# Kernel tuning notes

Measured on AMD Instinct MI355X. Metric: run time of the kernel, lower is better.

The kernel has to match this reference:

```python
import jax, jax.numpy as jnp
from jax import lax
import numpy as np
import math

NUM_CLASSES = 81
N_PER_IMG = 1024
NUM_IMAGES = 8
SCORE_THRESH = 0.05
NMS_THRESH = 0.5
DETS_PER_IMG = 100
WX, WY, WW, WH = 10.0, 10.0, 5.0, 5.0
BBOX_XFORM_CLIP = math.log(1000.0 / 16.0)


def setup_inputs() -> dict:
    key = jax.random.key(0)
    k1, k2, k3, k4 = jax.random.split(key, 4)
    M = NUM_IMAGES * N_PER_IMG
    H, W = 800, 1333
    class_logits = jax.random.normal(k1, (M, NUM_CLASSES), dtype=jnp.float32) * 3.0
    box_regression = jax.random.normal(k2, (M, 4 * NUM_CLASSES), dtype=jnp.float32) * 0.5
    # valid xyxy proposals inside the image
    xy1 = jax.random.uniform(k3, (M, 2), dtype=jnp.float32) * jnp.array([W * 0.7, H * 0.7], jnp.float32)
    wh = jax.random.uniform(k4, (M, 2), dtype=jnp.float32) * jnp.array([W * 0.3, H * 0.3], jnp.float32) + 4.0
    proposals = jnp.concatenate([xy1, xy1 + wh], axis=1)
    return {"class_logits": class_logits, "box_regression": box_regression,
            "proposals": proposals, "height": H, "width": W}


def _decode(rel_codes, boxes):
    widths = boxes[:, 2] - boxes[:, 0] + 1.0
    heights = boxes[:, 3] - boxes[:, 1] + 1.0
    ctr_x = boxes[:, 0] + 0.5 * widths
    ctr_y = boxes[:, 1] + 0.5 * heights
    rel = rel_codes.reshape(rel_codes.shape[0], -1, 4)  # [M, C, 4]
    dx = rel[:, :, 0] / WX
    dy = rel[:, :, 1] / WY
    dw = jnp.minimum(rel[:, :, 2] / WW, BBOX_XFORM_CLIP)
    dh = jnp.minimum(rel[:, :, 3] / WH, BBOX_XFORM_CLIP)
    pctr_x = dx * widths[:, None] + ctr_x[:, None]
    pctr_y = dy * heights[:, None] + ctr_y[:, None]
    pw = jnp.exp(dw) * widths[:, None]
    ph = jnp.exp(dh) * heights[:, None]
    return jnp.stack([pctr_x - 0.5 * pw, pctr_y - 0.5 * ph,
                      pctr_x + 0.5 * pw - 1.0, pctr_y + 0.5 * ph - 1.0], axis=-1)


def _clip(boxes, height, width):
    # boxes [..., 4] xyxy, clamp to [0, W-1] x [0, H-1]
    x = jnp.clip(boxes[..., 0::2], 0.0, float(width - 1))
    y = jnp.clip(boxes[..., 1::2], 0.0, float(height - 1))
    return jnp.stack([x[..., 0], y[..., 0], x[..., 1], y[..., 1]], axis=-1)


def _iou_matrix(b):
    x1, y1, x2, y2 = b[:, 0], b[:, 1], b[:, 2], b[:, 3]
    area = (x2 - x1 + 1.0) * (y2 - y1 + 1.0)
    xx1 = jnp.maximum(x1[:, None], x1[None, :])
    yy1 = jnp.maximum(y1[:, None], y1[None, :])
    xx2 = jnp.minimum(x2[:, None], x2[None, :])
    yy2 = jnp.minimum(y2[:, None], y2[None, :])
    inter = jnp.clip(xx2 - xx1 + 1.0, 0.0) * jnp.clip(yy2 - yy1 + 1.0, 0.0)
    return inter / (area[:, None] + area[None, :] - inter)


def _per_class(scores_j, boxes_j):
    # scores_j [N], boxes_j [N,4] -> sorted scores/boxes + greedy-NMS keep mask
    N = scores_j.shape[0]
    valid = scores_j > SCORE_THRESH
    s = jnp.where(valid, scores_j, 0.0)  # softmax scores are > 0
    order = jnp.argsort(-s)
    s_sorted = s[order]
    b_sorted = boxes_j[order]
    valid_sorted = valid[order]
    iou = _iou_matrix(b_sorted)  # [N, N]
    idxs = jnp.arange(N)

    def body(i, keep):
        sup = (iou[i] > NMS_THRESH) & keep[i] & (idxs > i)
        return keep & ~sup

    keep = lax.fori_loop(0, N, body, valid_sorted)
    return s_sorted, b_sorted, keep


def _per_image(prob_i, boxes_i):
    # prob_i [N, C], boxes_i [N, C, 4]; skip background class 0
    C = prob_i.shape[1]
    fg_scores = prob_i[:, 1:].T                      # [C-1, N]
    fg_boxes = jnp.swapaxes(boxes_i[:, 1:, :], 0, 1)  # [C-1, N, 4]
    s_sorted, b_sorted, keep = jax.vmap(_per_class)(fg_scores, fg_boxes)
    labels = jnp.broadcast_to(jnp.arange(1, C, dtype=jnp.int32)[:, None], s_sorted.shape)
    flat_s = jnp.where(keep, s_sorted, 0.0).reshape(-1)
    vals, idx = lax.top_k(flat_s, DETS_PER_IMG)      # detections-per-image limit
    boxes_out = b_sorted.reshape(-1, 4)[idx]
    labels_out = labels.reshape(-1)[idx]
    ok = vals > SCORE_THRESH
    return (jnp.where(ok, vals, 0.0),
            jnp.where(ok[:, None], boxes_out, 0.0),
            jnp.where(ok, labels_out, 0))


def reference(class_logits, box_regression, proposals, height, width):
    prob = jax.nn.softmax(class_logits, axis=-1)          # [M, C]
    dec = _decode(box_regression, proposals)              # [M, C, 4]
    dec = _clip(dec, height, width)
    B, N, C = NUM_IMAGES, N_PER_IMG, NUM_CLASSES
    prob = prob.reshape(B, N, C)
    dec = dec.reshape(B, N, C, 4)
    scores, boxes, labels = lax.map(lambda a: _per_image(a[0], a[1]), (prob, dec))
    return scores, boxes, labels
```

## Files before the change

kernel.cpp:

```cpp
#include <hip/hip_runtime.h>
#include <stdint.h>
#include <math.h>

#define NCLS 81
#define NFG  80
#define NPI  1024
#define NIMG 8
#define DETS 100
#define SCORE_T 0.05f
#define NMS_T   0.5f
#define NCAND   (NFG * DETS)
#define CAND_CAP 2048
#define FASTN 256
#define ROWS 64

static constexpr float BBOX_CLIP = 4.1351665567423557f;

__global__ __launch_bounds__(256) void softmax_probT(
    const float* __restrict__ logits, float* __restrict__ probT, int M)
{
    __shared__ float tile[ROWS * NCLS];
    __shared__ float mx[ROWS], dn[ROWS];
    int t = threadIdx.x;
    int rbase = blockIdx.x * ROWS;

    for (int idx = t; idx < ROWS * NCLS; idx += 256)
        tile[idx] = logits[(size_t)rbase * NCLS + idx];
    __syncthreads();

    if (t < ROWS) {
        const float* r = tile + t * NCLS;
        float m = r[0];
        #pragma unroll
        for (int j = 1; j < NCLS; ++j) m = fmaxf(m, r[j]);
        float s = 0.f;
        #pragma unroll
        for (int j = 0; j < NCLS; ++j) s += expf(r[j] - m);
        mx[t] = m; dn[t] = s;
    }
    __syncthreads();

    for (int o = t; o < ROWS * NFG; o += 256) {
        int r = o & 63;
        int c = o >> 6;
        float v = expf(tile[r * NCLS + (c + 1)] - mx[r]) / dn[r];
        probT[(size_t)c * M + rbase + r] = v;
    }
}

__global__ __launch_bounds__(256) void per_class_nms(
    const float* __restrict__ probT, const float* __restrict__ boxreg,
    const float* __restrict__ props, const int* __restrict__ hptr,
    const int* __restrict__ wptr, int* __restrict__ out_cnt,
    float* __restrict__ out_score, unsigned* __restrict__ out_key,
    float* __restrict__ out_box, int M)
{
    int pid = blockIdx.x;
    int img = pid / NFG;
    int c   = pid % NFG;
    int cls = c + 1;

    __shared__ float box_lds[NPI][4];
    __shared__ unsigned long long key[NPI];
    __shared__ int keep[NPI];
    __shared__ float sbox[FASTN][4];
    __shared__ float sarea[FASTN];
    __shared__ unsigned long long mask[FASTN][FASTN/64];
    __shared__ unsigned long long keepw[FASTN/64];
    __shared__ unsigned wpre[4];
    __shared__ int cnt;

    int t = threadIdx.x;
    float W1 = (float)(*wptr - 1);
    float H1 = (float)(*hptr - 1);

    if (t == 0) cnt = 0;
    for (int i = t; i < NPI; i += 256) key[i] = 0ULL;
    __syncthreads();

    {
        const float4 pv = *(const float4*)(probT + (size_t)c * M + img * NPI + 4 * t);
        float pr[4] = {pv.x, pv.y, pv.z, pv.w};
        #pragma unroll
        for (int j = 0; j < 4; ++j) {
            if (pr[j] > SCORE_T) {
                int m = 4 * t + j;
                int g = img * NPI + m;
                const float4 pb = *(const float4*)(props + (size_t)g * 4);
                float x1 = pb.x, y1 = pb.y, x2 = pb.z, y2 = pb.w;
                float w  = x2 - x1 + 1.0f, h = y2 - y1 + 1.0f;
                float cx = x1 + 0.5f * w,  cy = y1 + 0.5f * h;
                const float4 rc = *(const float4*)(boxreg + (size_t)g * (4 * NCLS) + 4 * cls);
                float dx = rc.x / 10.0f, dy = rc.y / 10.0f;
                float dw = fminf(rc.z / 5.0f, BBOX_CLIP);
                float dh = fminf(rc.w / 5.0f, BBOX_CLIP);
                float pcx = dx * w + cx, pcy = dy * h + cy;
                float pw = expf(dw) * w, ph = expf(dh) * h;
                float bx1 = pcx - 0.5f * pw;
                float by1 = pcy - 0.5f * ph;
                float bx2 = pcx + 0.5f * pw - 1.0f;
                float by2 = pcy + 0.5f * ph - 1.0f;
                bx1 = fminf(fmaxf(bx1, 0.f), W1);
                bx2 = fminf(fmaxf(bx2, 0.f), W1);
                by1 = fminf(fmaxf(by1, 0.f), H1);
                by2 = fminf(fmaxf(by2, 0.f), H1);
                box_lds[m][0] = bx1; box_lds[m][1] = by1;
                box_lds[m][2] = bx2; box_lds[m][3] = by2;
                int p = atomicAdd(&cnt, 1);
                unsigned fb = __float_as_uint(pr[j]);
                key[p] = ((unsigned long long)fb << 32) | (unsigned)(NPI - 1 - m);
            }
        }
    }
    __syncthreads();
    int n = cnt;

    if (n <= 64) {
        if (t < 64) {
            int lane = t;
            unsigned long long k = (lane < n) ? key[lane] : 0ULL;
            #pragma unroll
            for (int kk = 2; kk <= 64; kk <<= 1) {
                #pragma unroll
                for (int j = kk >> 1; j > 0; j >>= 1) {
                    unsigned long long o = __shfl_xor(k, j, 64);
                    bool up = ((lane & kk) == 0);
                    bool lower = ((lane & j) == 0);
                    bool take_max = (up == lower);
                    k = take_max ? (k > o ? k : o) : (k < o ? k : o);
                }
            }
            bool valid = (lane < n);
            float bx1 = 0.f, by1 = 0.f, bx2 = 0.f, by2 = 0.f, area = 0.f;
            if (valid) {
                int mi = NPI - 1 - (int)(k & 0xFFFFFFFFu);
                bx1 = box_lds[mi][0]; by1 = box_lds[mi][1];
                bx2 = box_lds[mi][2]; by2 = box_lds[mi][3];
                area = (bx2 - bx1 + 1.f) * (by2 - by1 + 1.f);
            }
            unsigned long long sup = 0ULL;
            for (int i = 0; i < n; ++i) {
                bool alive = !((sup >> i) & 1ULL);
                float ax1 = __shfl(bx1, i, 64), ay1 = __shfl(by1, i, 64);
                float ax2 = __shfl(bx2, i, 64), ay2 = __shfl(by2, i, 64);
                float aarea = __shfl(area, i, 64);
                bool s = false;
                if (alive && valid && lane > i) {
                    float xx1 = fmaxf(ax1, bx1), yy1 = fmaxf(ay1, by1);
                    float xx2 = fminf(ax2, bx2), yy2 = fminf(ay2, by2);
                    float iw = fmaxf(xx2 - xx1 + 1.f, 0.f);
                    float ih = fmaxf(yy2 - yy1 + 1.f, 0.f);
                    float inter = iw * ih;
                    float iou = inter / (aarea + area - inter);
                    s = iou > NMS_T;
                }
                sup |= __ballot(s);
            }
            bool kept = valid && !((sup >> lane) & 1ULL);
            unsigned long long keptm = __ballot(kept);
            int rank = __popcll(keptm & ((1ULL << lane) - 1ULL));
            if (kept && rank < DETS) {
                int slot = pid * DETS + rank;
                out_score[slot] = __uint_as_float((unsigned)(k >> 32));
                out_key[slot] = (unsigned)(c * NPI + lane);
                out_box[slot * 4 + 0] = bx1;
                out_box[slot * 4 + 1] = by1;
                out_box[slot * 4 + 2] = bx2;
                out_box[slot * 4 + 3] = by2;
            }
            if (lane == 0) {
                int tot = __popcll(keptm);
                out_cnt[pid] = tot < DETS ? tot : DETS;
            }
        }
        return;
    }

    int P = 2;
    while (P < n) P <<= 1;
    for (int k = 2; k <= P; k <<= 1) {
        for (int j = k >> 1; j > 0; j >>= 1) {
            for (int i = t; i < P; i += 256) {
                int ixj = i ^ j;
                if (ixj > i) {
                    unsigned long long a = key[i], b = key[ixj];
                    bool up = (i & k) == 0;
                    if (up ? (a < b) : (a > b)) { key[i] = b; key[ixj] = a; }
                }
            }
            __syncthreads();
        }
    }

    for (int i = t; i < NPI; i += 256) keep[i] = 0;
    __syncthreads();

    if (n <= FASTN) {
        for (int i = t; i < n; i += 256) {
            int mi = NPI - 1 - (int)(key[i] & 0xFFFFFFFFu);
            float bx1 = box_lds[mi][0], by1 = box_lds[mi][1];
            float bx2 = box_lds[mi][2], by2 = box_lds[mi][3];
            sbox[i][0] = bx1; sbox[i][1] = by1; sbox[i][2] = bx2; sbox[i][3] = by2;
            sarea[i] = (bx2 - bx1 + 1.f) * (by2 - by1 + 1.f);
        }
        __syncthreads();
        int nwords = ((n + 63) >> 6);
        for (int w = t; w < n * (FASTN/64); w += 256) {
            int i = w >> 2, wb = w & 3;
            if (wb >= nwords || ((wb + 1) << 6) - 1 <= i) { mask[i][wb] = 0ULL; continue; }
            float ax1 = sbox[i][0], ay1 = sbox[i][1];
            float ax2 = sbox[i][2], ay2 = sbox[i][3];
            float aarea = sarea[i];
            unsigned long long bits = 0ULL;
            int jbase = wb << 6;
            #pragma unroll 4
            for (int b = 0; b < 64; ++b) {
                int j = jbase + b;
                if (j < n && j > i) {
                    float bx1 = sbox[j][0], by1 = sbox[j][1];
                    float bx2 = sbox[j][2], by2 = sbox[j][3];
                    float xx1 = fmaxf(ax1, bx1), yy1 = fmaxf(ay1, by1);
                    float xx2 = fminf(ax2, bx2), yy2 = fminf(ay2, by2);
                    float iw = fmaxf(xx2 - xx1 + 1.f, 0.f);
                    float ih = fmaxf(yy2 - yy1 + 1.f, 0.f);
                    float inter = iw * ih;
                    float iou = inter / (aarea + sarea[j] - inter);
                    if (iou > NMS_T) bits |= (1ULL << b);
                }
            }
            mask[i][wb] = bits;
        }
        __syncthreads();
        if (t < 64) {
            int lane = t;
            unsigned long long kb = 0ULL;
            if (lane < 4) {
                int rem = n - (lane << 6);
                if (rem >= 64) kb = ~0ULL;
                else if (rem > 0) kb = (1ULL << rem) - 1ULL;
            }
            unsigned long long rm = 0ULL;
            for (int i = 0; i < n; ++i) {
                unsigned long long rw = __shfl(rm, i >> 6, 64);
                if (!((rw >> (i & 63)) & 1ULL)) {
                    unsigned long long mrow = (lane < 4) ? mask[i][lane] : 0ULL;
                    rm |= mrow;
                }
            }
            if (lane < 4) keepw[lane] = kb & ~rm;
        }
        __syncthreads();
        for (int i = t; i < n; i += 256)
            keep[i] = (int)((keepw[i >> 6] >> (i & 63)) & 1ULL);
        __syncthreads();
    } else {
        for (int i = t; i < n; i += 256) keep[i] = 1;
        __syncthreads();
        for (int i = 0; i < n; ++i) {
            if (keep[i]) {
                unsigned long long ki = key[i];
                int mi = NPI - 1 - (int)(ki & 0xFFFFFFFFu);
                float ax1 = box_lds[mi][0], ay1 = box_lds[mi][1];
                float ax2 = box_lds[mi][2], ay2 = box_lds[mi][3];
                float aarea = (ax2 - ax1 + 1.f) * (ay2 - ay1 + 1.f);
                for (int jj = i + 1 + t; jj < n; jj += 256) {
                    if (keep[jj]) {
                        int mj = NPI - 1 - (int)(key[jj] & 0xFFFFFFFFu);
                        float bx1 = box_lds[mj][0], by1 = box_lds[mj][1];
                        float bx2 = box_lds[mj][2], by2 = box_lds[mj][3];
                        float xx1 = fmaxf(ax1, bx1), yy1 = fmaxf(ay1, by1);
                        float xx2 = fminf(ax2, bx2), yy2 = fminf(ay2, by2);
                        float iw = fmaxf(xx2 - xx1 + 1.f, 0.f);
                        float ih = fmaxf(yy2 - yy1 + 1.f, 0.f);
                        float inter = iw * ih;
                        float barea = (bx2 - bx1 + 1.f) * (by2 - by1 + 1.f);
                        float iou = inter / (aarea + barea - inter);
                        if (iou > NMS_T) keep[jj] = 0;
                    }
                }
            }
            __syncthreads();
        }
    }

    {
        int lane = t & 63, w = t >> 6;
        int k0 = keep[4 * t], k1 = keep[4 * t + 1];
        int k2 = keep[4 * t + 2], k3 = keep[4 * t + 3];
        unsigned s = (unsigned)(k0 + k1 + k2 + k3);
        unsigned v = s;
        #pragma unroll
        for (int off = 1; off < 64; off <<= 1) {
            unsigned u = __shfl_up(v, off, 64);
            v += (lane >= off) ? u : 0u;
        }
        if (lane == 63) wpre[w] = v;
        __syncthreads();
        unsigned woff = 0;
        for (int w2 = 0; w2 < w; ++w2) woff += wpre[w2];
        unsigned before = v + woff - s;
        unsigned r = before;
        #pragma unroll
        for (int j = 0; j < 4; ++j) {
            int i = 4 * t + j;
            int kv = (j == 0) ? k0 : (j == 1) ? k1 : (j == 2) ? k2 : k3;
            if (kv && r < DETS) {
                unsigned long long ki = key[i];
                int mi = NPI - 1 - (int)(ki & 0xFFFFFFFFu);
                int slot = pid * DETS + (int)r;
                out_score[slot] = __uint_as_float((unsigned)(ki >> 32));
                out_key[slot] = (unsigned)(c * NPI + i);
                out_box[slot * 4 + 0] = box_lds[mi][0];
                out_box[slot * 4 + 1] = box_lds[mi][1];
                out_box[slot * 4 + 2] = box_lds[mi][2];
                out_box[slot * 4 + 3] = box_lds[mi][3];
            }
            r += (unsigned)kv;
        }
        __syncthreads();
        if (t == 0) {
            unsigned tot = wpre[0] + wpre[1] + wpre[2] + wpre[3];
            out_cnt[pid] = (int)(tot < DETS ? tot : DETS);
        }
    }
}

__device__ __forceinline__ void suffix_select(
    unsigned* hist, unsigned* wtot, int K, int* outB, unsigned* outAbove)
{
    int t = threadIdx.x, lane = t & 63, w = t >> 6;
    unsigned c0 = hist[4 * t], c1 = hist[4 * t + 1];
    unsigned c2 = hist[4 * t + 2], c3 = hist[4 * t + 3];
    unsigned ps = c0 + c1 + c2 + c3;
    unsigned v = ps;
    #pragma unroll
    for (int off = 1; off < 64; off <<= 1) {
        unsigned u = __shfl_down(v, off, 64);
        v += (lane + off < 64) ? u : 0u;
    }
    if (lane == 0) wtot[w] = v;
    __syncthreads();
    unsigned woff = 0;
    for (int w2 = w + 1; w2 < 16; ++w2) woff += wtot[w2];
    unsigned Sown = v + woff;
    unsigned A3 = Sown - ps;
    unsigned A2 = A3 + c3, A1 = A2 + c2, A0 = A1 + c1;
    unsigned A[4] = {A0, A1, A2, A3};
    unsigned C[4] = {c0, c1, c2, c3};
    #pragma unroll
    for (int j = 0; j < 4; ++j) {
        if ((int)A[j] < K && (int)(A[j] + C[j]) >= K) {
            *outB = 4 * t + j;
            *outAbove = A[j];
        }
    }
    __syncthreads();
}

__global__ __launch_bounds__(1024) void topk_merge(
    const int* __restrict__ cnts, const float* __restrict__ escore,
    const unsigned* __restrict__ ekey, const float* __restrict__ ebox,
    float* __restrict__ out)
{
    int img = blockIdx.x;
    __shared__ unsigned sc[NCAND];
    __shared__ unsigned hist[4096];
    __shared__ unsigned long long cand[CAND_CAP];
    __shared__ unsigned wtot[16];
    __shared__ int sB1, sB2, sNc;
    __shared__ unsigned sAb1, sAb2;

    int t = threadIdx.x;
    if (t == 0) { sB1 = 0; sB2 = 0; sNc = 0; sAb1 = 0; sAb2 = 0; }
    for (int p = t; p < NCAND; p += 1024) {
        int cc = p / DETS, k = p % DETS;
        unsigned fb = 0;
        if (k < cnts[img * NFG + cc]) fb = __float_as_uint(escore[img * NCAND + p]);
        sc[p] = fb;
    }
    for (int i = t; i < 4096; i += 1024) hist[i] = 0;
    __syncthreads();

    for (int p = t; p < NCAND; p += 1024) {
        unsigned fb = sc[p];
        if (fb) atomicAdd(&hist[fb >> 19], 1u);
    }
    __syncthreads();
    suffix_select(hist, wtot, DETS, &sB1, &sAb1);
    int B1 = sB1;
    unsigned ab1 = sAb1;

    for (int i = t; i < 4096; i += 1024) hist[i] = 0;
    __syncthreads();
    for (int p = t; p < NCAND; p += 1024) {
        unsigned fb = sc[p];
        if (fb && (int)(fb >> 19) == B1) atomicAdd(&hist[(fb >> 7) & 0xFFFu], 1u);
    }
    __syncthreads();
    suffix_select(hist, wtot, DETS - (int)ab1, &sB2, &sAb2);
    int B2 = sB2;

    for (int p = t; p < NCAND; p += 1024) {
        unsigned fb = sc[p];
        if (fb) {
            int d1 = (int)(fb >> 19);
            bool ok = d1 > B1 || (d1 == B1 && (int)((fb >> 7) & 0xFFFu) >= B2);
            if (ok) {
                int pos = atomicAdd(&sNc, 1);
                if (pos < CAND_CAP) {
                    unsigned fk = ekey[img * NCAND + p];
                    unsigned low = ((0x1FFFFu - fk) << 13) | (unsigned)p;
                    cand[pos] = ((unsigned long long)fb << 32) | low;
                }
            }
        }
    }
    __syncthreads();
    int nc = sNc < CAND_CAP ? sNc : CAND_CAP;
    int P = 128;
    while (P < nc) P <<= 1;
    for (int i = t; i < P; i += 1024)
        if (i >= nc) cand[i] = 0ULL;
    __syncthreads();

    for (int k = 2; k <= P; k <<= 1) {
        for (int j = k >> 1; j > 0; j >>= 1) {
            for (int i = t; i < P; i += 1024) {
                int ixj = i ^ j;
                if (ixj > i) {
                    unsigned long long a = cand[i], b = cand[ixj];
                    bool up = (i & k) == 0;
                    if (up ? (a < b) : (a > b)) { cand[i] = b; cand[ixj] = a; }
                }
            }
            __syncthreads();
        }
    }

    float* oScore = out;
    float* oBox   = out + NIMG * DETS;
    float* oLab   = out + NIMG * DETS * 5;

    if (t < DETS) {
        unsigned long long b = cand[t];
        int o = img * DETS + t;
        if (b != 0ULL) {
            float scv = __uint_as_float((unsigned)(b >> 32));
            unsigned low = (unsigned)(b & 0xFFFFFFFFu);
            unsigned flatkey = 0x1FFFFu - ((low >> 13) & 0x1FFFFu);
            int p = (int)(low & 0x1FFFu);
            int gp = img * NCAND + p;
            oScore[o] = scv;
            oBox[o * 4 + 0] = ebox[gp * 4 + 0];
            oBox[o * 4 + 1] = ebox[gp * 4 + 1];
            oBox[o * 4 + 2] = ebox[gp * 4 + 2];
            oBox[o * 4 + 3] = ebox[gp * 4 + 3];
            oLab[o] = (float)((flatkey >> 10) + 1);
        } else {
            oScore[o] = 0.f;
            oBox[o * 4 + 0] = 0.f; oBox[o * 4 + 1] = 0.f;
            oBox[o * 4 + 2] = 0.f; oBox[o * 4 + 3] = 0.f;
            oLab[o] = 0.f;
        }
    }
}

extern "C" void kernel_launch(void* const* d_in, const int* in_sizes, int n_in,
                              void* d_out, int out_size, void* d_ws, size_t ws_size,
                              hipStream_t stream) {
    const float* logits = (const float*)d_in[0];
    const float* boxreg = (const float*)d_in[1];
    const float* props  = (const float*)d_in[2];
    const int*   hptr   = (const int*)d_in[3];
    const int*   wptr   = (const int*)d_in[4];
    float* out = (float*)d_out;
    int M = in_sizes[0] / NCLS;

    char* ws = (char*)d_ws;
    float*    probT  = (float*)ws;    ws += (size_t)NFG * M * sizeof(float);
    int*      cnt    = (int*)ws;      ws += (size_t)NIMG * NFG * sizeof(int);
    float*    escore = (float*)ws;    ws += (size_t)NIMG * NCAND * sizeof(float);
    unsigned* ekey   = (unsigned*)ws; ws += (size_t)NIMG * NCAND * sizeof(unsigned);
    float*    ebox   = (float*)ws;    ws += (size_t)NIMG * NCAND * 4 * sizeof(float);

    softmax_probT<<<M / ROWS, 256, 0, stream>>>(logits, probT, M);
    per_class_nms<<<NIMG * NFG, 256, 0, stream>>>(
        probT, boxreg, props, hptr, wptr, cnt, escore, ekey, ebox, M);
    topk_merge<<<NIMG, 1024, 0, stream>>>(cnt, escore, ekey, ebox, out);
}
```

Measured before the change: 61.07 us.

## Replace bitonic sorts with rank-by-counting sorts in NMS and top-k merge

Both the per-class key sort in the NMS kernel and the candidate sort in the merge kernel become O(n^2) rank-counting sorts: each thread counts how many keys beat its own and scatters to that rank. This removes the log^2 stages of __syncthreads-bound bitonic passes. The merge kernel also drops to 256 threads, uses a 16-bins-per-thread suffix scan, fuses the score load with the histogram, and halves the candidate cap. The quadratic counting can cost more when n is large (up to 1024 per class), and the smaller cap risks truncating candidates when many scores tie.

```diff
diff --git a/kernel.cpp b/kernel.cpp
--- a/kernel.cpp
+++ b/kernel.cpp
@@ -10,7 +10,7 @@
 #define SCORE_T 0.05f
 #define NMS_T   0.5f
 #define NCAND   (NFG * DETS)
-#define CAND_CAP 2048
+#define CAND_CAP 1024
 #define FASTN 256
 #define ROWS 64
 
@@ -23,11 +23,9 @@
     __shared__ float mx[ROWS], dn[ROWS];
     int t = threadIdx.x;
     int rbase = blockIdx.x * ROWS;
-
     for (int idx = t; idx < ROWS * NCLS; idx += 256)
         tile[idx] = logits[(size_t)rbase * NCLS + idx];
     __syncthreads();
-
     if (t < ROWS) {
         const float* r = tile + t * NCLS;
         float m = r[0];
@@ -39,14 +37,24 @@
         mx[t] = m; dn[t] = s;
     }
     __syncthreads();
-
     for (int o = t; o < ROWS * NFG; o += 256) {
         int r = o & 63;
         int c = o >> 6;
-        float v = expf(tile[r * NCLS + (c + 1)] - mx[r]) / dn[r];
-        probT[(size_t)c * M + rbase + r] = v;
+        probT[(size_t)c * M + rbase + r] = expf(tile[r * NCLS + (c + 1)] - mx[r]) / dn[r];
     }
 }
+
+struct ShP2 {
+    float box[NPI][4];
+    unsigned long long key[NPI];
+    unsigned long long skey[NPI];
+    int keep[NPI];
+    float sbox[FASTN][4];
+    float sarea[FASTN];
+    unsigned long long mask[FASTN][FASTN/64];
+    unsigned long long keepw[FASTN/64];
+    unsigned wpre[4];
+};
 
 __global__ __launch_bounds__(256) void per_class_nms(
     const float* __restrict__ probT, const float* __restrict__ boxreg,
@@ -60,22 +68,13 @@
     int c   = pid % NFG;
     int cls = c + 1;
 
-    __shared__ float box_lds[NPI][4];
-    __shared__ unsigned long long key[NPI];
-    __shared__ int keep[NPI];
-    __shared__ float sbox[FASTN][4];
-    __shared__ float sarea[FASTN];
-    __shared__ unsigned long long mask[FASTN][FASTN/64];
-    __shared__ unsigned long long keepw[FASTN/64];
-    __shared__ unsigned wpre[4];
+    __shared__ ShP2 sp;
     __shared__ int cnt;
-
     int t = threadIdx.x;
     float W1 = (float)(*wptr - 1);
     float H1 = (float)(*hptr - 1);
 
     if (t == 0) cnt = 0;
-    for (int i = t; i < NPI; i += 256) key[i] = 0ULL;
     __syncthreads();
 
     {
@@ -96,19 +95,15 @@
                 float dh = fminf(rc.w / 5.0f, BBOX_CLIP);
                 float pcx = dx * w + cx, pcy = dy * h + cy;
                 float pw = expf(dw) * w, ph = expf(dh) * h;
-                float bx1 = pcx - 0.5f * pw;
-                float by1 = pcy - 0.5f * ph;
-                float bx2 = pcx + 0.5f * pw - 1.0f;
-                float by2 = pcy + 0.5f * ph - 1.0f;
-                bx1 = fminf(fmaxf(bx1, 0.f), W1);
-                bx2 = fminf(fmaxf(bx2, 0.f), W1);
-                by1 = fminf(fmaxf(by1, 0.f), H1);
-                by2 = fminf(fmaxf(by2, 0.f), H1);
-                box_lds[m][0] = bx1; box_lds[m][1] = by1;
-                box_lds[m][2] = bx2; box_lds[m][3] = by2;
+                float bx1 = fminf(fmaxf(pcx - 0.5f * pw, 0.f), W1);
+                float by1 = fminf(fmaxf(pcy - 0.5f * ph, 0.f), H1);
+                float bx2 = fminf(fmaxf(pcx + 0.5f * pw - 1.0f, 0.f), W1);
+                float by2 = fminf(fmaxf(pcy + 0.5f * ph - 1.0f, 0.f), H1);
+                sp.box[m][0] = bx1; sp.box[m][1] = by1;
+                sp.box[m][2] = bx2; sp.box[m][3] = by2;
                 int p = atomicAdd(&cnt, 1);
-                unsigned fb = __float_as_uint(pr[j]);
-                key[p] = ((unsigned long long)fb << 32) | (unsigned)(NPI - 1 - m);
+                sp.key[p] = ((unsigned long long)__float_as_uint(pr[j]) << 32)
+                          | (unsigned)(NPI - 1 - m);
             }
         }
     }
@@ -118,15 +113,13 @@
     if (n <= 64) {
         if (t < 64) {
             int lane = t;
-            unsigned long long k = (lane < n) ? key[lane] : 0ULL;
+            unsigned long long k = (lane < n) ? sp.key[lane] : 0ULL;
             #pragma unroll
             for (int kk = 2; kk <= 64; kk <<= 1) {
                 #pragma unroll
                 for (int j = kk >> 1; j > 0; j >>= 1) {
                     unsigned long long o = __shfl_xor(k, j, 64);
-                    bool up = ((lane & kk) == 0);
-                    bool lower = ((lane & j) == 0);
-                    bool take_max = (up == lower);
+                    bool take_max = (((lane & kk) == 0) == ((lane & j) == 0));
                     k = take_max ? (k > o ? k : o) : (k < o ? k : o);
                 }
             }
@@ -134,8 +127,8 @@
             float bx1 = 0.f, by1 = 0.f, bx2 = 0.f, by2 = 0.f, area = 0.f;
             if (valid) {
                 int mi = NPI - 1 - (int)(k & 0xFFFFFFFFu);
-                bx1 = box_lds[mi][0]; by1 = box_lds[mi][1];
-                bx2 = box_lds[mi][2]; by2 = box_lds[mi][3];
+                bx1 = sp.box[mi][0]; by1 = sp.box[mi][1];
+                bx2 = sp.box[mi][2]; by2 = sp.box[mi][3];
                 area = (bx2 - bx1 + 1.f) * (by2 - by1 + 1.f);
             }
             unsigned long long sup = 0ULL;
@@ -151,8 +144,7 @@
                     float iw = fmaxf(xx2 - xx1 + 1.f, 0.f);
                     float ih = fmaxf(yy2 - yy1 + 1.f, 0.f);
                     float inter = iw * ih;
-                    float iou = inter / (aarea + area - inter);
-                    s = iou > NMS_T;
+                    s = inter / (aarea + area - inter) > NMS_T;
                 }
                 sup |= __ballot(s);
             }
@@ -163,10 +155,8 @@
                 int slot = pid * DETS + rank;
                 out_score[slot] = __uint_as_float((unsigned)(k >> 32));
                 out_key[slot] = (unsigned)(c * NPI + lane);
-                out_box[slot * 4 + 0] = bx1;
-                out_box[slot * 4 + 1] = by1;
-                out_box[slot * 4 + 2] = bx2;
-                out_box[slot * 4 + 3] = by2;
+                out_box[slot * 4 + 0] = bx1; out_box[slot * 4 + 1] = by1;
+                out_box[slot * 4 + 2] = bx2; out_box[slot * 4 + 3] = by2;
             }
             if (lane == 0) {
                 int tot = __popcll(keptm);
@@ -176,59 +166,49 @@
         return;
     }
 
-    int P = 2;
-    while (P < n) P <<= 1;
-    for (int k = 2; k <= P; k <<= 1) {
-        for (int j = k >> 1; j > 0; j >>= 1) {
-            for (int i = t; i < P; i += 256) {
-                int ixj = i ^ j;
-                if (ixj > i) {
-                    unsigned long long a = key[i], b = key[ixj];
-                    bool up = (i & k) == 0;
-                    if (up ? (a < b) : (a > b)) { key[i] = b; key[ixj] = a; }
-                }
-            }
-            __syncthreads();
-        }
-    }
-
-    for (int i = t; i < NPI; i += 256) keep[i] = 0;
+    for (int i = t; i < NPI; i += 256) sp.keep[i] = 0;
+    for (int i = t; i < n; i += 256) {
+        unsigned long long ki = sp.key[i];
+        int r = 0;
+        for (int j = 0; j < n; ++j) r += (sp.key[j] > ki) ? 1 : 0;
+        sp.skey[r] = ki;
+    }
     __syncthreads();
 
     if (n <= FASTN) {
         for (int i = t; i < n; i += 256) {
-            int mi = NPI - 1 - (int)(key[i] & 0xFFFFFFFFu);
-            float bx1 = box_lds[mi][0], by1 = box_lds[mi][1];
-            float bx2 = box_lds[mi][2], by2 = box_lds[mi][3];
-            sbox[i][0] = bx1; sbox[i][1] = by1; sbox[i][2] = bx2; sbox[i][3] = by2;
-            sarea[i] = (bx2 - bx1 + 1.f) * (by2 - by1 + 1.f);
+            int mi = NPI - 1 - (int)(sp.skey[i] & 0xFFFFFFFFu);
+            float bx1 = sp.box[mi][0], by1 = sp.box[mi][1];
+            float bx2 = sp.box[mi][2], by2 = sp.box[mi][3];
+            sp.sbox[i][0] = bx1; sp.sbox[i][1] = by1;
+            sp.sbox[i][2] = bx2; sp.sbox[i][3] = by2;
+            sp.sarea[i] = (bx2 - bx1 + 1.f) * (by2 - by1 + 1.f);
         }
         __syncthreads();
         int nwords = ((n + 63) >> 6);
         for (int w = t; w < n * (FASTN/64); w += 256) {
             int i = w >> 2, wb = w & 3;
-            if (wb >= nwords || ((wb + 1) << 6) - 1 <= i) { mask[i][wb] = 0ULL; continue; }
-            float ax1 = sbox[i][0], ay1 = sbox[i][1];
-            float ax2 = sbox[i][2], ay2 = sbox[i][3];
-            float aarea = sarea[i];
+            if (wb >= nwords || ((wb + 1) << 6) - 1 <= i) { sp.mask[i][wb] = 0ULL; continue; }
+            float ax1 = sp.sbox[i][0], ay1 = sp.sbox[i][1];
+            float ax2 = sp.sbox[i][2], ay2 = sp.sbox[i][3];
+            float aarea = sp.sarea[i];
             unsigned long long bits = 0ULL;
             int jbase = wb << 6;
             #pragma unroll 4
             for (int b = 0; b < 64; ++b) {
                 int j = jbase + b;
                 if (j < n && j > i) {
-                    float bx1 = sbox[j][0], by1 = sbox[j][1];
-                    float bx2 = sbox[j][2], by2 = sbox[j][3];
+                    float bx1 = sp.sbox[j][0], by1 = sp.sbox[j][1];
+                    float bx2 = sp.sbox[j][2], by2 = sp.sbox[j][3];
                     float xx1 = fmaxf(ax1, bx1), yy1 = fmaxf(ay1, by1);
                     float xx2 = fminf(ax2, bx2), yy2 = fminf(ay2, by2);
                     float iw = fmaxf(xx2 - xx1 + 1.f, 0.f);
                     float ih = fmaxf(yy2 - yy1 + 1.f, 0.f);
                     float inter = iw * ih;
-                    float iou = inter / (aarea + sarea[j] - inter);
-                    if (iou > NMS_T) bits |= (1ULL << b);
-                }
-            }
-            mask[i][wb] = bits;
+                    if (inter / (aarea + sp.sarea[j] - inter) > NMS_T) bits |= (1ULL << b);
+                }
+            }
+            sp.mask[i][wb] = bits;
         }
         __syncthreads();
         if (t < 64) {
@@ -243,39 +223,38 @@
             for (int i = 0; i < n; ++i) {
                 unsigned long long rw = __shfl(rm, i >> 6, 64);
                 if (!((rw >> (i & 63)) & 1ULL)) {
-                    unsigned long long mrow = (lane < 4) ? mask[i][lane] : 0ULL;
+                    unsigned long long mrow = (lane < 4) ? sp.mask[i][lane] : 0ULL;
                     rm |= mrow;
                 }
             }
-            if (lane < 4) keepw[lane] = kb & ~rm;
+            if (lane < 4) sp.keepw[lane] = kb & ~rm;
         }
         __syncthreads();
         for (int i = t; i < n; i += 256)
-            keep[i] = (int)((keepw[i >> 6] >> (i & 63)) & 1ULL);
+            sp.keep[i] = (int)((sp.keepw[i >> 6] >> (i & 63)) & 1ULL);
         __syncthreads();
     } else {
-        for (int i = t; i < n; i += 256) keep[i] = 1;
+        for (int i = t; i < n; i += 256) sp.keep[i] = 1;
         __syncthreads();
         for (int i = 0; i < n; ++i) {
-            if (keep[i]) {
-                unsigned long long ki = key[i];
+            if (sp.keep[i]) {
+                unsigned long long ki = sp.skey[i];
                 int mi = NPI - 1 - (int)(ki & 0xFFFFFFFFu);
-                float ax1 = box_lds[mi][0], ay1 = box_lds[mi][1];
-                float ax2 = box_lds[mi][2], ay2 = box_lds[mi][3];
+                float ax1 = sp.box[mi][0], ay1 = sp.box[mi][1];
+                float ax2 = sp.box[mi][2], ay2 = sp.box[mi][3];
                 float aarea = (ax2 - ax1 + 1.f) * (ay2 - ay1 + 1.f);
                 for (int jj = i + 1 + t; jj < n; jj += 256) {
-                    if (keep[jj]) {
-                        int mj = NPI - 1 - (int)(key[jj] & 0xFFFFFFFFu);
-                        float bx1 = box_lds[mj][0], by1 = box_lds[mj][1];
-                        float bx2 = box_lds[mj][2], by2 = box_lds[mj][3];
+                    if (sp.keep[jj]) {
+                        int mj = NPI - 1 - (int)(sp.skey[jj] & 0xFFFFFFFFu);
+                        float bx1 = sp.box[mj][0], by1 = sp.box[mj][1];
+                        float bx2 = sp.box[mj][2], by2 = sp.box[mj][3];
                         float xx1 = fmaxf(ax1, bx1), yy1 = fmaxf(ay1, by1);
                         float xx2 = fminf(ax2, bx2), yy2 = fminf(ay2, by2);
                         float iw = fmaxf(xx2 - xx1 + 1.f, 0.f);
                         float ih = fmaxf(yy2 - yy1 + 1.f, 0.f);
                         float inter = iw * ih;
                         float barea = (bx2 - bx1 + 1.f) * (by2 - by1 + 1.f);
-                        float iou = inter / (aarea + barea - inter);
-                        if (iou > NMS_T) keep[jj] = 0;
+                        if (inter / (aarea + barea - inter) > NMS_T) sp.keep[jj] = 0;
                     }
                 }
             }
@@ -285,8 +264,8 @@
 
     {
         int lane = t & 63, w = t >> 6;
-        int k0 = keep[4 * t], k1 = keep[4 * t + 1];
-        int k2 = keep[4 * t + 2], k3 = keep[4 * t + 3];
+        int k0 = sp.keep[4 * t], k1 = sp.keep[4 * t + 1];
+        int k2 = sp.keep[4 * t + 2], k3 = sp.keep[4 * t + 3];
         unsigned s = (unsigned)(k0 + k1 + k2 + k3);
         unsigned v = s;
         #pragma unroll
@@ -294,44 +273,43 @@
             unsigned u = __shfl_up(v, off, 64);
             v += (lane >= off) ? u : 0u;
         }
-        if (lane == 63) wpre[w] = v;
+        if (lane == 63) sp.wpre[w] = v;
         __syncthreads();
         unsigned woff = 0;
-        for (int w2 = 0; w2 < w; ++w2) woff += wpre[w2];
-        unsigned before = v + woff - s;
-        unsigned r = before;
+        for (int w2 = 0; w2 < w; ++w2) woff += sp.wpre[w2];
+        unsigned r = v + woff - s;
         #pragma unroll
         for (int j = 0; j < 4; ++j) {
             int i = 4 * t + j;
             int kv = (j == 0) ? k0 : (j == 1) ? k1 : (j == 2) ? k2 : k3;
             if (kv && r < DETS) {
-                unsigned long long ki = key[i];
+                unsigned long long ki = sp.skey[i];
                 int mi = NPI - 1 - (int)(ki & 0xFFFFFFFFu);
                 int slot = pid * DETS + (int)r;
                 out_score[slot] = __uint_as_float((unsigned)(ki >> 32));
                 out_key[slot] = (unsigned)(c * NPI + i);
-                out_box[slot * 4 + 0] = box_lds[mi][0];
-                out_box[slot * 4 + 1] = box_lds[mi][1];
-                out_box[slot * 4 + 2] = box_lds[mi][2];
-                out_box[slot * 4 + 3] = box_lds[mi][3];
+                out_box[slot * 4 + 0] = sp.box[mi][0];
+                out_box[slot * 4 + 1] = sp.box[mi][1];
+                out_box[slot * 4 + 2] = sp.box[mi][2];
+                out_box[slot * 4 + 3] = sp.box[mi][3];
             }
             r += (unsigned)kv;
         }
         __syncthreads();
         if (t == 0) {
-            unsigned tot = wpre[0] + wpre[1] + wpre[2] + wpre[3];
+            unsigned tot = sp.wpre[0] + sp.wpre[1] + sp.wpre[2] + sp.wpre[3];
             out_cnt[pid] = (int)(tot < DETS ? tot : DETS);
         }
     }
 }
 
-__device__ __forceinline__ void suffix_select(
+__device__ __forceinline__ void suffix_select256(
     unsigned* hist, unsigned* wtot, int K, int* outB, unsigned* outAbove)
 {
     int t = threadIdx.x, lane = t & 63, w = t >> 6;
-    unsigned c0 = hist[4 * t], c1 = hist[4 * t + 1];
-    unsigned c2 = hist[4 * t + 2], c3 = hist[4 * t + 3];
-    unsigned ps = c0 + c1 + c2 + c3;
+    unsigned loc[16]; unsigned ps = 0;
+    #pragma unroll
+    for (int j = 0; j < 16; ++j) { loc[j] = hist[t * 16 + j]; ps += loc[j]; }
     unsigned v = ps;
     #pragma unroll
     for (int off = 1; off < 64; off <<= 1) {
@@ -341,23 +319,19 @@
     if (lane == 0) wtot[w] = v;
     __syncthreads();
     unsigned woff = 0;
-    for (int w2 = w + 1; w2 < 16; ++w2) woff += wtot[w2];
-    unsigned Sown = v + woff;
-    unsigned A3 = Sown - ps;
-    unsigned A2 = A3 + c3, A1 = A2 + c2, A0 = A1 + c1;
-    unsigned A[4] = {A0, A1, A2, A3};
-    unsigned C[4] = {c0, c1, c2, c3};
+    for (int w2 = w + 1; w2 < 4; ++w2) woff += wtot[w2];
+    unsigned base = v + woff - ps;
+    unsigned suf = 0;
     #pragma unroll
-    for (int j = 0; j < 4; ++j) {
-        if ((int)A[j] < K && (int)(A[j] + C[j]) >= K) {
-            *outB = 4 * t + j;
-            *outAbove = A[j];
-        }
+    for (int j = 15; j >= 0; --j) {
+        unsigned A = base + suf;
+        if ((int)A < K && (int)(A + loc[j]) >= K) { *outB = t * 16 + j; *outAbove = A; }
+        suf += loc[j];
     }
     __syncthreads();
 }
 
-__global__ __launch_bounds__(1024) void topk_merge(
+__global__ __launch_bounds__(256) void topk_merge(
     const int* __restrict__ cnts, const float* __restrict__ escore,
     const unsigned* __restrict__ ekey, const float* __restrict__ ebox,
     float* __restrict__ out)
@@ -366,41 +340,38 @@
     __shared__ unsigned sc[NCAND];
     __shared__ unsigned hist[4096];
     __shared__ unsigned long long cand[CAND_CAP];
-    __shared__ unsigned wtot[16];
+    __shared__ int scnts[NFG];
+    __shared__ unsigned wtot[4];
     __shared__ int sB1, sB2, sNc;
     __shared__ unsigned sAb1, sAb2;
 
     int t = threadIdx.x;
+    if (t < NFG) scnts[t] = cnts[img * NFG + t];
     if (t == 0) { sB1 = 0; sB2 = 0; sNc = 0; sAb1 = 0; sAb2 = 0; }
-    for (int p = t; p < NCAND; p += 1024) {
-        int cc = p / DETS, k = p % DETS;
+    for (int i = t; i < 4096; i += 256) hist[i] = 0;
+    __syncthreads();
+
+    for (int p = t; p < NCAND; p += 256) {
         unsigned fb = 0;
-        if (k < cnts[img * NFG + cc]) fb = __float_as_uint(escore[img * NCAND + p]);
+        if ((p % DETS) < scnts[p / DETS]) fb = __float_as_uint(escore[img * NCAND + p]);
         sc[p] = fb;
-    }
-    for (int i = t; i < 4096; i += 1024) hist[i] = 0;
-    __syncthreads();
-
-    for (int p = t; p < NCAND; p += 1024) {
-        unsigned fb = sc[p];
         if (fb) atomicAdd(&hist[fb >> 19], 1u);
     }
     __syncthreads();
-    suffix_select(hist, wtot, DETS, &sB1, &sAb1);
-    int B1 = sB1;
-    unsigned ab1 = sAb1;
-
-    for (int i = t; i < 4096; i += 1024) hist[i] = 0;
-    __syncthreads();
-    for (int p = t; p < NCAND; p += 1024) {
+    suffix_select256(hist, wtot, DETS, &sB1, &sAb1);
+    int B1 = sB1; unsigned ab1 = sAb1;
+
+    for (int i = t; i < 4096; i += 256) hist[i] = 0;
+    __syncthreads();
+    for (int p = t; p < NCAND; p += 256) {
         unsigned fb = sc[p];
         if (fb && (int)(fb >> 19) == B1) atomicAdd(&hist[(fb >> 7) & 0xFFFu], 1u);
     }
     __syncthreads();
-    suffix_select(hist, wtot, DETS - (int)ab1, &sB2, &sAb2);
+    suffix_select256(hist, wtot, DETS - (int)ab1, &sB2, &sAb2);
     int B2 = sB2;
 
-    for (int p = t; p < NCAND; p += 1024) {
+    for (int p = t; p < NCAND; p += 256) {
         unsigned fb = sc[p];
         if (fb) {
             int d1 = (int)(fb >> 19);
@@ -409,58 +380,46 @@
                 int pos = atomicAdd(&sNc, 1);
                 if (pos < CAND_CAP) {
                     unsigned fk = ekey[img * NCAND + p];
-                    unsigned low = ((0x1FFFFu - fk) << 13) | (unsigned)p;
-                    cand[pos] = ((unsigned long long)fb << 32) | low;
+                    cand[pos] = ((unsigned long long)fb << 32)
+                              | (((0x1FFFFu - fk) << 13) | (unsigned)p);
                 }
             }
         }
     }
     __syncthreads();
     int nc = sNc < CAND_CAP ? sNc : CAND_CAP;
-    int P = 128;
-    while (P < nc) P <<= 1;
-    for (int i = t; i < P; i += 1024)
-        if (i >= nc) cand[i] = 0ULL;
-    __syncthreads();
-
-    for (int k = 2; k <= P; k <<= 1) {
-        for (int j = k >> 1; j > 0; j >>= 1) {
-            for (int i = t; i < P; i += 1024) {
-                int ixj = i ^ j;
-                if (ixj > i) {
-                    unsigned long long a = cand[i], b = cand[ixj];
-                    bool up = (i & k) == 0;
-                    if (up ? (a < b) : (a > b)) { cand[i] = b; cand[ixj] = a; }
-                }
-            }
-            __syncthreads();
-        }
-    }
 
     float* oScore = out;
     float* oBox   = out + NIMG * DETS;
     float* oLab   = out + NIMG * DETS * 5;
 
-    if (t < DETS) {
-        unsigned long long b = cand[t];
-        int o = img * DETS + t;
-        if (b != 0ULL) {
-            float scv = __uint_as_float((unsigned)(b >> 32));
-            unsigned low = (unsigned)(b & 0xFFFFFFFFu);
+    for (int k = t; k < DETS; k += 256) {
+        if (k >= nc) {
+            int o = img * DETS + k;
+            oScore[o] = 0.f;
+            oBox[o * 4 + 0] = 0.f; oBox[o * 4 + 1] = 0.f;
+            oBox[o * 4 + 2] = 0.f; oBox[o * 4 + 3] = 0.f;
+            oLab[o] = 0.f;
+        }
+    }
+
+    for (int i = t; i < nc; i += 256) {
+        unsigned long long ki = cand[i];
+        int r = 0;
+        for (int j = 0; j < nc; ++j) r += (cand[j] > ki) ? 1 : 0;
+        if (r < DETS) {
+            float scv = __uint_as_float((unsigned)(ki >> 32));
+            unsigned low = (unsigned)(ki & 0xFFFFFFFFu);
             unsigned flatkey = 0x1FFFFu - ((low >> 13) & 0x1FFFFu);
             int p = (int)(low & 0x1FFFu);
             int gp = img * NCAND + p;
+            int o = img * DETS + r;
             oScore[o] = scv;
             oBox[o * 4 + 0] = ebox[gp * 4 + 0];
             oBox[o * 4 + 1] = ebox[gp * 4 + 1];
             oBox[o * 4 + 2] = ebox[gp * 4 + 2];
             oBox[o * 4 + 3] = ebox[gp * 4 + 3];
             oLab[o] = (float)((flatkey >> 10) + 1);
-        } else {
-            oScore[o] = 0.f;
-            oBox[o * 4 + 0] = 0.f; oBox[o * 4 + 1] = 0.f;
-            oBox[o * 4 + 2] = 0.f; oBox[o * 4 + 3] = 0.f;
-            oLab[o] = 0.f;
         }
     }
 }
@@ -478,13 +437,13 @@
 
     char* ws = (char*)d_ws;
     float*    probT  = (float*)ws;    ws += (size_t)NFG * M * sizeof(float);
-    int*      cnt    = (int*)ws;      ws += (size_t)NIMG * NFG * sizeof(int);
+    int*      gcnt   = (int*)ws;      ws += (size_t)NIMG * NFG * sizeof(int);
     float*    escore = (float*)ws;    ws += (size_t)NIMG * NCAND * sizeof(float);
     unsigned* ekey   = (unsigned*)ws; ws += (size_t)NIMG * NCAND * sizeof(unsigned);
     float*    ebox   = (float*)ws;    ws += (size_t)NIMG * NCAND * 4 * sizeof(float);
 
     softmax_probT<<<M / ROWS, 256, 0, stream>>>(logits, probT, M);
     per_class_nms<<<NIMG * NFG, 256, 0, stream>>>(
-        probT, boxreg, props, hptr, wptr, cnt, escore, ekey, ebox, M);
-    topk_merge<<<NIMG, 1024, 0, stream>>>(cnt, escore, ekey, ebox, out);
+        probT, boxreg, props, hptr, wptr, gcnt, escore, ekey, ebox, M);
+    topk_merge<<<NIMG, 256, 0, stream>>>(gcnt, escore, ekey, ebox, out);
 }
```

Result: slower. 66.43 us (+8.8%).
